# Kernel optimization log

Hardware: AMD Instinct MI355X
Metric: run time of the kernel (lower is better)

## Reference

```python
import jax, jax.numpy as jnp
import numpy as np

B, Q, C_IN, C_OUT, S, NH = 4, 4096, 256, 256, 8, 8
H_FEAT, W_FEAT = 128, 128


def grid_sample_bilinear(img, grid):
    """torch.nn.functional.grid_sample, mode='bilinear', padding_mode='zeros', align_corners=False.
    img: [B, C, H, W]; grid: [B, Hg, Wg, 2] with (x, y) in [-1, 1]. Returns [B, C, Hg, Wg]."""
    b, c, h, w = img.shape
    gx = (grid[..., 0] + 1.0) * (w * 0.5) - 0.5
    gy = (grid[..., 1] + 1.0) * (h * 0.5) - 0.5
    x0f = jnp.floor(gx)
    y0f = jnp.floor(gy)
    x0 = x0f.astype(jnp.int32)
    y0 = y0f.astype(jnp.int32)
    wx1 = (gx - x0f)[:, None]  # [B,1,Hg,Wg]
    wy1 = (gy - y0f)[:, None]
    img_flat = img.reshape(b, c, h * w)

    def corner(xi, yi):
        inb = ((xi >= 0) & (xi < w) & (yi >= 0) & (yi < h)).astype(img.dtype)
        idx = jnp.clip(yi, 0, h - 1) * w + jnp.clip(xi, 0, w - 1)
        v = jax.vmap(lambda im, ix: im[:, ix.reshape(-1)])(img_flat, idx)  # [B,C,Hg*Wg]
        return v.reshape(b, c, *xi.shape[1:]) * inb[:, None]

    v00 = corner(x0, y0)
    v01 = corner(x0 + 1, y0)
    v10 = corner(x0, y0 + 1)
    v11 = corner(x0 + 1, y0 + 1)
    return (v00 * (1 - wx1) * (1 - wy1) + v01 * wx1 * (1 - wy1)
            + v10 * (1 - wx1) * wy1 + v11 * wx1 * wy1)


def setup_inputs() -> dict:
    key = jax.random.key(0)
    ks = jax.random.split(key, 16)
    sc = 0.02
    return {
        "queries": jax.random.normal(ks[0], (B, Q, C_IN), jnp.float32),
        "keys": jax.random.normal(ks[1], (B, C_IN, H_FEAT, W_FEAT), jnp.float32),
        "values": jax.random.normal(ks[2], (B, C_IN, H_FEAT, W_FEAT), jnp.float32),
        "W_loc": jax.random.normal(ks[3], (C_IN, S * 2), jnp.float32) * sc,
        "b_loc": jnp.zeros((S * 2,), jnp.float32),
        "W_q": jax.random.normal(ks[4], (C_IN, C_OUT), jnp.float32) * sc,
        "b_q": jnp.zeros((C_OUT,), jnp.float32),
        "W_k": jax.random.normal(ks[5], (C_OUT, C_IN), jnp.float32) * sc,
        "b_k": jnp.zeros((C_OUT,), jnp.float32),
        "W_v": jax.random.normal(ks[6], (C_OUT, C_IN), jnp.float32) * sc,
        "b_v": jnp.zeros((C_OUT,), jnp.float32),
        "W_o": jax.random.normal(ks[7], (C_OUT, C_OUT), jnp.float32) * sc,
        "b_o": jnp.zeros((C_OUT,), jnp.float32),
    }


def reference(queries, keys, values, W_loc, b_loc, W_q, b_q, W_k, b_k, W_v, b_v, W_o, b_o):
    b, q, _ = queries.shape
    d = C_OUT // NH
    # predicted sampling locations in [-1, 1]: [B, Q, S, 2]
    loc = jnp.tanh(queries @ W_loc + b_loc).reshape(b, q, S, 2)
    # query projection -> [B, Q, NH, d]
    qh = (queries @ W_q + b_q).reshape(b, q, NH, d)
    # 1x1 conv projections of feature maps
    k_proj = jnp.einsum('oc,bchw->bohw', W_k, keys) + b_k[None, :, None, None]
    v_proj = jnp.einsum('oc,bchw->bohw', W_v, values) + b_v[None, :, None, None]
    # deformable sampling: [B, C_OUT, Q, S] -> [B, Q, NH, d, S]
    ks_ = grid_sample_bilinear(k_proj, loc).transpose(0, 2, 1, 3).reshape(b, q, NH, d, S)
    vs_ = grid_sample_bilinear(v_proj, loc).transpose(0, 2, 1, 3).reshape(b, q, NH, d, S)
    # per-query attention over S sampled points (note: scale uses full out_channels)
    attn = jnp.einsum('bqhd,bqhds->bqhs', qh, ks_) / np.sqrt(C_OUT).astype(np.float32)
    attn = jax.nn.softmax(attn, axis=-1)
    out = jnp.einsum('bqhds,bqhs->bqhd', vs_, attn).reshape(b, q, C_OUT)
    return out @ W_o + b_o
```

## Files before the change

kernel.cpp:

```cpp
#include <hip/hip_runtime.h>
#include <hip/hip_bf16.h>

#define NB 4
#define NQ 4096
#define CI 256
#define CO 256
#define NS 8
#define HFEAT 128
#define WFEAT 128
#define NPIX (HFEAT * WFEAT)

typedef short bf16x8 __attribute__((ext_vector_type(8)));
typedef float f32x4 __attribute__((ext_vector_type(4)));

__device__ __forceinline__ unsigned short f2b(float x) {
    union { float f; unsigned u; } v; v.f = x;
    unsigned r = v.u + 0x7fff + ((v.u >> 16) & 1);
    return (unsigned short)(r >> 16);
}
__device__ __forceinline__ float b2f(unsigned short x) {
    union { unsigned u; float f; } v; v.u = ((unsigned)x) << 16;
    return v.f;
}
__device__ __forceinline__ void b2f2(unsigned u, float& a, float& b) {
    union { unsigned x; float f; } va, vb;
    va.x = u << 16;
    vb.x = u & 0xffff0000u;
    a = va.f; b = vb.f;
}
__device__ __forceinline__ void gload16(const void* g, void* l) {
    __builtin_amdgcn_global_load_lds((const __attribute__((address_space(1))) void*)g,
                                     (__attribute__((address_space(3))) void*)l, 16, 0, 0);
}

__global__ __launch_bounds__(256) void k_prep_w(const float* __restrict__ Wk,
                                                const float* __restrict__ Wv,
                                                const float* __restrict__ Wq,
                                                const float* __restrict__ Wo,
                                                unsigned short* __restrict__ out) {
    int mat = blockIdx.y;
    int base = blockIdx.x * 1024 + threadIdx.x * 4;
    const float* src = (mat == 0) ? Wk : (mat == 1) ? Wv : (mat == 2) ? Wq : Wo;
    unsigned short* dst = out + (size_t)mat * 65536;
    if (mat < 2) {
#pragma unroll
        for (int i = 0; i < 4; ++i) dst[base + i] = f2b(src[base + i]);
    } else {
#pragma unroll
        for (int i = 0; i < 4; ++i) {
            int oi = base + i;
            int o = oi >> 8, c = oi & 255;
            dst[oi] = f2b(src[c * 256 + o]);
        }
    }
}

__global__ __launch_bounds__(256) void k_cvt(const float* __restrict__ in,
                                             unsigned short* __restrict__ out) {
    size_t i = ((size_t)blockIdx.x * 256 + threadIdx.x) * 8;
    float4 a = *reinterpret_cast<const float4*>(in + i);
    float4 b = *reinterpret_cast<const float4*>(in + i + 4);
    union { uint2 u2[2]; unsigned short h[8]; } pk;
    pk.h[0] = f2b(a.x); pk.h[1] = f2b(a.y); pk.h[2] = f2b(a.z); pk.h[3] = f2b(a.w);
    pk.h[4] = f2b(b.x); pk.h[5] = f2b(b.y); pk.h[6] = f2b(b.z); pk.h[7] = f2b(b.w);
    *reinterpret_cast<uint4*>(out + i) = *reinterpret_cast<uint4*>(&pk);
}

__global__ __launch_bounds__(256) void k_loc(const float* __restrict__ q,
                                             const float* __restrict__ Wl,
                                             const float* __restrict__ bl,
                                             float* __restrict__ loc) {
    __shared__ float qs[32][260];
    __shared__ float wlt[16][260];
    int t = threadIdx.x;
    int row0 = blockIdx.x * 32;
    {
        int rr = t >> 6;
        int c4 = (t & 63) * 4;
#pragma unroll
        for (int i = 0; i < 8; ++i) {
            int r = i * 4 + rr;
            *reinterpret_cast<float4*>(&qs[r][c4]) =
                *reinterpret_cast<const float4*>(q + (size_t)(row0 + r) * CI + c4);
        }
    }
    {
        int c = t;
#pragma unroll
        for (int col = 0; col < 16; ++col) wlt[col][c] = Wl[c * 16 + col];
    }
    __syncthreads();
    int r = t & 31;
    int cg = t >> 5;
    float a0 = bl[cg], a1 = bl[cg + 8];
    for (int c4 = 0; c4 < 256; c4 += 4) {
        float4 qv = *reinterpret_cast<const float4*>(&qs[r][c4]);
        float4 w0 = *reinterpret_cast<const float4*>(&wlt[cg][c4]);
        float4 w1 = *reinterpret_cast<const float4*>(&wlt[cg + 8][c4]);
        a0 = fmaf(qv.x, w0.x, a0); a0 = fmaf(qv.y, w0.y, a0);
        a0 = fmaf(qv.z, w0.z, a0); a0 = fmaf(qv.w, w0.w, a0);
        a1 = fmaf(qv.x, w1.x, a1); a1 = fmaf(qv.y, w1.y, a1);
        a1 = fmaf(qv.z, w1.z, a1); a1 = fmaf(qv.w, w1.w, a1);
    }
    loc[(size_t)(row0 + r) * 16 + cg] = tanhf(a0);
    loc[(size_t)(row0 + r) * 16 + cg + 8] = tanhf(a1);
}

template <int OUT_BF16>
__global__ __launch_bounds__(256) void k_gemm(const unsigned short* __restrict__ A,
                                              const unsigned short* __restrict__ Bt,
                                              const float* __restrict__ bias,
                                              void* __restrict__ outp) {
    __shared__ unsigned short As[128][32];
    __shared__ unsigned short Bs[128][32];
    int t = threadIdx.x;
    int w = t >> 6, l = t & 63;
    int bm = blockIdx.x >> 1, bc = blockIdx.x & 1;
    int m0 = bm * 128, n0 = bc * 128;
    int wr = w >> 1, wc = w & 1;

    f32x4 acc[4][4];
#pragma unroll
    for (int n = 0; n < 4; ++n) {
        float bv = bias[n0 + wc * 64 + n * 16 + (l & 15)];
#pragma unroll
        for (int m = 0; m < 4; ++m) acc[m][n] = f32x4{bv, bv, bv, bv};
    }

    int ar = wr * 64 + (l & 15);
    int br = wc * 64 + (l & 15);
    int kq = (l >> 4) * 8;
    int srow = (l >> 2);
    int scol = (l & 3) * 8;

    for (int kk = 0; kk < 8; ++kk) {
        int k0 = kk * 32;
#pragma unroll
        for (int j = 0; j < 2; ++j) {
            int row = w * 32 + j * 16 + srow;
            gload16(A + (size_t)(m0 + row) * CI + k0 + scol, &As[w * 32 + j * 16][0]);
            gload16(Bt + (size_t)(n0 + row) * CI + k0 + scol, &Bs[w * 32 + j * 16][0]);
        }
        __syncthreads();
        bf16x8 af[4], bfr[4];
#pragma unroll
        for (int m = 0; m < 4; ++m) af[m] = *reinterpret_cast<const bf16x8*>(&As[ar + m * 16][kq]);
#pragma unroll
        for (int n = 0; n < 4; ++n) bfr[n] = *reinterpret_cast<const bf16x8*>(&Bs[br + n * 16][kq]);
#pragma unroll
        for (int m = 0; m < 4; ++m)
#pragma unroll
            for (int n = 0; n < 4; ++n)
                acc[m][n] = __builtin_amdgcn_mfma_f32_16x16x32_bf16(af[m], bfr[n], acc[m][n], 0, 0, 0);
        __syncthreads();
    }

    int rbase = m0 + wr * 64 + (l >> 4) * 4;
    int cbase = n0 + wc * 64 + (l & 15);
#pragma unroll
    for (int m = 0; m < 4; ++m)
#pragma unroll
        for (int n = 0; n < 4; ++n)
#pragma unroll
            for (int r = 0; r < 4; ++r) {
                size_t row = rbase + m * 16 + r;
                size_t col = cbase + n * 16;
                if (OUT_BF16)
                    ((unsigned short*)outp)[row * CO + col] = f2b(acc[m][n][r]);
                else
                    ((float*)outp)[row * CO + col] = acc[m][n][r];
            }
}

__global__ __launch_bounds__(256) void k_proj(const float* __restrict__ keys,
                                              const float* __restrict__ values,
                                              const unsigned short* __restrict__ wbuf,
                                              const float* __restrict__ bK,
                                              const float* __restrict__ bV,
                                              unsigned short* __restrict__ kp,
                                              unsigned short* __restrict__ vp) {
    __shared__ unsigned short As[128][40];
    __shared__ unsigned short Bs[128][32];
    int blk = ((blockIdx.x & 7) << 8) | (blockIdx.x >> 3);
    int map = blk >> 10;
    int rem = blk & 1023;
    int b = rem >> 8;
    int rem2 = rem & 255;
    int pix0 = (rem2 >> 1) * 128;
    int o0 = (rem2 & 1) * 128;
    const float* X = (map ? values : keys) + (size_t)b * (CI * NPIX);
    const unsigned short* W = wbuf + (size_t)map * 65536;
    const float* bias = map ? bV : bK;
    unsigned short* outp = (map ? vp : kp) + (size_t)b * (NPIX * CO);

    int t = threadIdx.x;
    int w = t >> 6, l = t & 63;
    int wr = w >> 1, wc = w & 1;

    f32x4 acc[4][4];
#pragma unroll
    for (int n = 0; n < 4; ++n) {
        float bv = bias[o0 + wc * 64 + n * 16 + (l & 15)];
#pragma unroll
        for (int m = 0; m < 4; ++m) acc[m][n] = f32x4{bv, bv, bv, bv};
    }

    int srow = l >> 2, scol = (l & 3) * 8;
    int pl = t & 31;
    int ch = (t >> 5) * 2;
    int ar = wr * 64 + (l & 15);
    int br = wc * 64 + (l & 15);
    int kq = (l >> 4) * 8;

    for (int kk = 0; kk < 8; ++kk) {
        int k0 = kk * 32;
#pragma unroll
        for (int j = 0; j < 2; ++j) {
            int row = w * 32 + j * 16 + srow;
            gload16(W + (size_t)(o0 + row) * CI + k0 + scol, &Bs[w * 32 + j * 16][0]);
        }
        float v0[2][4], v1[2][4];
#pragma unroll
        for (int i = 0; i < 2; ++i) {
            const float* xr0 = X + (size_t)(k0 + i * 16 + ch) * NPIX + pix0 + pl;
            const float* xr1 = xr0 + NPIX;
#pragma unroll
            for (int j = 0; j < 4; ++j) {
                v0[i][j] = xr0[j * 32];
                v1[i][j] = xr1[j * 32];
            }
        }
#pragma unroll
        for (int i = 0; i < 2; ++i)
#pragma unroll
            for (int j = 0; j < 4; ++j) {
                unsigned pkd = (unsigned)f2b(v0[i][j]) | ((unsigned)f2b(v1[i][j]) << 16);
                *reinterpret_cast<unsigned*>(&As[pl + j * 32][i * 16 + ch]) = pkd;
            }
        __syncthreads();
        bf16x8 af[4], bfr[4];
#pragma unroll
        for (int m = 0; m < 4; ++m) af[m] = *reinterpret_cast<const bf16x8*>(&As[ar + m * 16][kq]);
#pragma unroll
        for (int n = 0; n < 4; ++n) bfr[n] = *reinterpret_cast<const bf16x8*>(&Bs[br + n * 16][kq]);
#pragma unroll
        for (int m = 0; m < 4; ++m)
#pragma unroll
            for (int n = 0; n < 4; ++n)
                acc[m][n] = __builtin_amdgcn_mfma_f32_16x16x32_bf16(af[m], bfr[n], acc[m][n], 0, 0, 0);
        __syncthreads();
    }

    int rbase = wr * 64 + (l >> 4) * 4;
    int cbase = o0 + wc * 64 + (l & 15);
#pragma unroll
    for (int m = 0; m < 4; ++m)
#pragma unroll
        for (int n = 0; n < 4; ++n)
#pragma unroll
            for (int r = 0; r < 4; ++r) {
                size_t row = (size_t)pix0 + rbase + m * 16 + r;
                size_t col = cbase + n * 16;
                outp[row * CO + col] = f2b(acc[m][n][r]);
            }
}

__global__ __launch_bounds__(256) void k_attn(const unsigned short* __restrict__ kp,
                                              const unsigned short* __restrict__ vp,
                                              const unsigned short* __restrict__ qh,
                                              const float* __restrict__ loc,
                                              unsigned short* __restrict__ aout) {
    int t = threadIdx.x;
    int wv = t >> 6, l = t & 63;
    int blk = blockIdx.x;
    int xcd = blk & 7;
    int b = xcd >> 1;
    int idx = ((blk >> 3) << 1) | (xcd & 1);
    int bq = (b << 12) | (idx << 2) | wv;

    float qv[4];
    {
        uint2 qr = *reinterpret_cast<const uint2*>(qh + (size_t)bq * CO + l * 4);
        b2f2(qr.x, qv[0], qv[1]);
        b2f2(qr.y, qv[2], qv[3]);
    }
    const unsigned short* kb = kp + (size_t)b * NPIX * CO;
    const unsigned short* vb = vp + (size_t)b * NPIX * CO;
    const float* lq = loc + (size_t)bq * (NS * 2);
    int choff = l * 4;

    float m = -3.0e38f, lsum = 0.f;
    float o0 = 0.f, o1 = 0.f, o2 = 0.f, o3 = 0.f;

#pragma unroll
    for (int s = 0; s < NS; ++s) {
        float x = lq[2 * s];
        float y = lq[2 * s + 1];
        float gx = (x + 1.f) * (WFEAT * 0.5f) - 0.5f;
        float gy = (y + 1.f) * (HFEAT * 0.5f) - 0.5f;
        float x0f = floorf(gx), y0f = floorf(gy);
        int x0 = (int)x0f, y0 = (int)y0f;
        float wx1 = gx - x0f, wy1 = gy - y0f;
        float wx0 = 1.f - wx1, wy0 = 1.f - wy1;
        bool xa = (x0 >= 0) && (x0 < WFEAT);
        bool xb = (x0 + 1 >= 0) && (x0 + 1 < WFEAT);
        bool ya = (y0 >= 0) && (y0 < HFEAT);
        bool yb = (y0 + 1 >= 0) && (y0 + 1 < HFEAT);
        size_t i00 = (size_t)(y0 * WFEAT + x0) * CO + choff;

        uint2 z = make_uint2(0u, 0u);
        uint2 k00 = z, k01 = z, k10 = z, k11 = z;
        uint2 v00 = z, v01 = z, v10 = z, v11 = z;
        if (xa && ya) { k00 = *(const uint2*)(kb + i00);                 v00 = *(const uint2*)(vb + i00); }
        if (xb && ya) { k01 = *(const uint2*)(kb + i00 + CO);            v01 = *(const uint2*)(vb + i00 + CO); }
        if (xa && yb) { k10 = *(const uint2*)(kb + i00 + WFEAT * CO);    v10 = *(const uint2*)(vb + i00 + WFEAT * CO); }
        if (xb && yb) { k11 = *(const uint2*)(kb + i00 + (WFEAT+1)*CO);  v11 = *(const uint2*)(vb + i00 + (WFEAT+1)*CO); }

        float a0, a1, b0, b1, c0, c1, d0, d1;
        float ks[4], vs[4];
        b2f2(k00.x, a0, a1); b2f2(k01.x, b0, b1); b2f2(k10.x, c0, c1); b2f2(k11.x, d0, d1);
        ks[0] = fmaf(fmaf(b0, wx1, a0 * wx0), wy0, fmaf(d0, wx1, c0 * wx0) * wy1);
        ks[1] = fmaf(fmaf(b1, wx1, a1 * wx0), wy0, fmaf(d1, wx1, c1 * wx0) * wy1);
        b2f2(k00.y, a0, a1); b2f2(k01.y, b0, b1); b2f2(k10.y, c0, c1); b2f2(k11.y, d0, d1);
        ks[2] = fmaf(fmaf(b0, wx1, a0 * wx0), wy0, fmaf(d0, wx1, c0 * wx0) * wy1);
        ks[3] = fmaf(fmaf(b1, wx1, a1 * wx0), wy0, fmaf(d1, wx1, c1 * wx0) * wy1);
        b2f2(v00.x, a0, a1); b2f2(v01.x, b0, b1); b2f2(v10.x, c0, c1); b2f2(v11.x, d0, d1);
        vs[0] = fmaf(fmaf(b0, wx1, a0 * wx0), wy0, fmaf(d0, wx1, c0 * wx0) * wy1);
        vs[1] = fmaf(fmaf(b1, wx1, a1 * wx0), wy0, fmaf(d1, wx1, c1 * wx0) * wy1);
        b2f2(v00.y, a0, a1); b2f2(v01.y, b0, b1); b2f2(v10.y, c0, c1); b2f2(v11.y, d0, d1);
        vs[2] = fmaf(fmaf(b0, wx1, a0 * wx0), wy0, fmaf(d0, wx1, c0 * wx0) * wy1);
        vs[3] = fmaf(fmaf(b1, wx1, a1 * wx0), wy0, fmaf(d1, wx1, c1 * wx0) * wy1);

        float p = fmaf(qv[0], ks[0], fmaf(qv[1], ks[1], fmaf(qv[2], ks[2], qv[3] * ks[3])));
        p += __shfl_xor(p, 1);
        p += __shfl_xor(p, 2);
        p += __shfl_xor(p, 4);
        float lg = p * 0.0625f;

        float nm = fmaxf(m, lg);
        float sc = __expf(m - nm);
        float wgt = __expf(lg - nm);
        lsum = fmaf(lsum, sc, wgt);
        o0 = fmaf(o0, sc, wgt * vs[0]);
        o1 = fmaf(o1, sc, wgt * vs[1]);
        o2 = fmaf(o2, sc, wgt * vs[2]);
        o3 = fmaf(o3, sc, wgt * vs[3]);
        m = nm;
    }

    float inv = 1.f / lsum;
    uint2 pk;
    pk.x = ((unsigned)f2b(o0 * inv)) | (((unsigned)f2b(o1 * inv)) << 16);
    pk.y = ((unsigned)f2b(o2 * inv)) | (((unsigned)f2b(o3 * inv)) << 16);
    *reinterpret_cast<uint2*>(aout + (size_t)bq * CO + choff) = pk;
}

extern "C" void kernel_launch(void* const* d_in, const int* in_sizes, int n_in,
                              void* d_out, int out_size, void* d_ws, size_t ws_size,
                              hipStream_t stream) {
    (void)in_sizes; (void)n_in; (void)out_size; (void)ws_size;
    const float* queries = (const float*)d_in[0];
    const float* keys    = (const float*)d_in[1];
    const float* values  = (const float*)d_in[2];
    const float* W_loc   = (const float*)d_in[3];
    const float* b_loc   = (const float*)d_in[4];
    const float* W_q     = (const float*)d_in[5];
    const float* b_q     = (const float*)d_in[6];
    const float* W_k     = (const float*)d_in[7];
    const float* b_k     = (const float*)d_in[8];
    const float* W_v     = (const float*)d_in[9];
    const float* b_v     = (const float*)d_in[10];
    const float* W_o     = (const float*)d_in[11];
    const float* b_o     = (const float*)d_in[12];
    float* out = (float*)d_out;

    char* ws = (char*)d_ws;
    unsigned short* kp   = (unsigned short*)(ws);
    unsigned short* vp   = (unsigned short*)(ws + 33554432);
    unsigned short* qbf  = (unsigned short*)(ws + 67108864);
    unsigned short* aout = (unsigned short*)(ws + 67108864);
    unsigned short* qh   = (unsigned short*)(ws + 75497472);
    float* locb          = (float*)(ws + 83886080);
    unsigned short* wbuf = (unsigned short*)(ws + 84934656);

    k_prep_w<<<dim3(64, 4), 256, 0, stream>>>(W_k, W_v, W_q, W_o, wbuf);
    k_cvt<<<dim3(2048), 256, 0, stream>>>(queries, qbf);
    k_loc<<<dim3(512), 256, 0, stream>>>(queries, W_loc, b_loc, locb);
    k_gemm<1><<<dim3(256), 256, 0, stream>>>(qbf, wbuf + 131072, b_q, qh);
    k_proj<<<dim3(2048), 256, 0, stream>>>(keys, values, wbuf, b_k, b_v, kp, vp);
    k_attn<<<dim3(NB * NQ / 4), 256, 0, stream>>>(kp, vp, qh, locb, aout);
    k_gemm<0><<<dim3(256), 256, 0, stream>>>(aout, wbuf + 196608, b_o, out);
}
```

Measured before the change: 128.3 us.

## Software-pipeline projection GEMM loads with double-buffered B tile and swizzled A layout

```diff
diff --git a/kernel.cpp b/kernel.cpp
--- a/kernel.cpp
+++ b/kernel.cpp
@@ -180,7 +180,7 @@
                                               unsigned short* __restrict__ kp,
                                               unsigned short* __restrict__ vp) {
     __shared__ unsigned short As[128][40];
-    __shared__ unsigned short Bs[128][32];
+    __shared__ unsigned short Bs[2][128][32];
     int blk = ((blockIdx.x & 7) << 8) | (blockIdx.x >> 3);
     int map = blk >> 10;
     int rem = blk & 1023;
@@ -205,50 +205,86 @@
         for (int m = 0; m < 4; ++m) acc[m][n] = f32x4{bv, bv, bv, bv};
     }
 
+    int cp0 = t >> 5;
+    int pxl = 4 * (t & 31);
+    int fx = ((t & 31) ^ ((t & 31) >> 2)) & 3;
+    int colA = cp0 ^ (fx << 2);
+    int colB = (cp0 + 8) ^ (fx << 2);
+    const float* Xp = X + pix0 + pxl;
+
     int srow = l >> 2, scol = (l & 3) * 8;
-    int pl = t & 31;
-    int ch = (t >> 5) * 2;
+
     int ar = wr * 64 + (l & 15);
     int br = wc * 64 + (l & 15);
-    int kq = (l >> 4) * 8;
+    int g = l >> 4;
+    int kq = g * 8;
+
+    float4 fa0, fa1, fa2, fa3;
+
+#define LOADA(kk)                                                         \
+    {                                                                     \
+        const float* p_ = Xp + (size_t)((kk) * 32 + 2 * cp0) * NPIX;      \
+        fa0 = *(const float4*)(p_);                                       \
+        fa1 = *(const float4*)(p_ + NPIX);                                \
+        fa2 = *(const float4*)(p_ + 16 * NPIX);                           \
+        fa3 = *(const float4*)(p_ + 17 * NPIX);                           \
+    }
+#define WRITEA()                                                          \
+    {                                                                     \
+        const float* q0_ = (const float*)&fa0;                            \
+        const float* q1_ = (const float*)&fa1;                            \
+        const float* q2_ = (const float*)&fa2;                            \
+        const float* q3_ = (const float*)&fa3;                            \
+        _Pragma("unroll")                                                 \
+        for (int j = 0; j < 4; ++j) {                                     \
+            unsigned d0_ = (unsigned)f2b(q0_[j]) | ((unsigned)f2b(q1_[j]) << 16); \
+            unsigned d1_ = (unsigned)f2b(q2_[j]) | ((unsigned)f2b(q3_[j]) << 16); \
+            unsigned* rp_ = (unsigned*)&As[pxl + j][0];                   \
+            rp_[colA] = d0_;                                              \
+            rp_[colB] = d1_;                                              \
+        }                                                                 \
+    }
+#define LOADB(kk, buf)                                                    \
+    {                                                                     \
+        int k0_ = (kk) * 32;                                              \
+        _Pragma("unroll")                                                 \
+        for (int j = 0; j < 2; ++j) {                                     \
+            int row_ = w * 32 + j * 16;                                   \
+            gload16(W + (size_t)(o0 + row_ + srow) * CI + k0_ + scol,     \
+                    &Bs[buf][row_][0]);                                   \
+        }                                                                 \
+    }
+
+    LOADA(0);
+    LOADB(0, 0);
+    WRITEA();
+    __syncthreads();
 
     for (int kk = 0; kk < 8; ++kk) {
-        int k0 = kk * 32;
-#pragma unroll
-        for (int j = 0; j < 2; ++j) {
-            int row = w * 32 + j * 16 + srow;
-            gload16(W + (size_t)(o0 + row) * CI + k0 + scol, &Bs[w * 32 + j * 16][0]);
-        }
-        float v0[2][4], v1[2][4];
-#pragma unroll
-        for (int i = 0; i < 2; ++i) {
-            const float* xr0 = X + (size_t)(k0 + i * 16 + ch) * NPIX + pix0 + pl;
-            const float* xr1 = xr0 + NPIX;
-#pragma unroll
-            for (int j = 0; j < 4; ++j) {
-                v0[i][j] = xr0[j * 32];
-                v1[i][j] = xr1[j * 32];
-            }
-        }
-#pragma unroll
-        for (int i = 0; i < 2; ++i)
-#pragma unroll
-            for (int j = 0; j < 4; ++j) {
-                unsigned pkd = (unsigned)f2b(v0[i][j]) | ((unsigned)f2b(v1[i][j]) << 16);
-                *reinterpret_cast<unsigned*>(&As[pl + j * 32][i * 16 + ch]) = pkd;
-            }
-        __syncthreads();
+        if (kk < 7) {
+            LOADA(kk + 1);
+            LOADB(kk + 1, (kk + 1) & 1);
+        }
         bf16x8 af[4], bfr[4];
 #pragma unroll
-        for (int m = 0; m < 4; ++m) af[m] = *reinterpret_cast<const bf16x8*>(&As[ar + m * 16][kq]);
-#pragma unroll
-        for (int n = 0; n < 4; ++n) bfr[n] = *reinterpret_cast<const bf16x8*>(&Bs[br + n * 16][kq]);
+        for (int m = 0; m < 4; ++m) {
+            int p = ar + m * 16;
+            int gm = (g ^ (((p >> 2) ^ (p >> 4)) & 3)) * 8;
+            af[m] = *reinterpret_cast<const bf16x8*>(&As[p][gm]);
+        }
+#pragma unroll
+        for (int n = 0; n < 4; ++n)
+            bfr[n] = *reinterpret_cast<const bf16x8*>(&Bs[kk & 1][br + n * 16][kq]);
 #pragma unroll
         for (int m = 0; m < 4; ++m)
 #pragma unroll
             for (int n = 0; n < 4; ++n)
                 acc[m][n] = __builtin_amdgcn_mfma_f32_16x16x32_bf16(af[m], bfr[n], acc[m][n], 0, 0, 0);
         __syncthreads();
+        if (kk < 7) {
+            WRITEA();
+            __syncthreads();
+        }
     }
 
     int rbase = wr * 64 + (l >> 4) * 4;
@@ -263,6 +299,9 @@
                 size_t col = cbase + n * 16;
                 outp[row * CO + col] = f2b(acc[m][n][r]);
             }
+#undef LOADA
+#undef WRITEA
+#undef LOADB
 }
 
 __global__ __launch_bounds__(256) void k_attn(const unsigned short* __restrict__ kp,
```

New measurement: 124.2 us. 3.1% less time.

## Restructure k_proj to stage full-K pixel tile once and reuse across both output halves

Applied to the files above, without the earlier changes.

```diff
diff --git a/kernel.cpp b/kernel.cpp
--- a/kernel.cpp
+++ b/kernel.cpp
@@ -27,6 +27,11 @@
     va.x = u << 16;
     vb.x = u & 0xffff0000u;
     a = va.f; b = vb.f;
+}
+__device__ __forceinline__ unsigned cvtpk(float a, float b) {
+    unsigned r;
+    asm("v_cvt_pk_bf16_f32 %0, %1, %2" : "=v"(r) : "v"(a), "v"(b));
+    return r;
 }
 __device__ __forceinline__ void gload16(const void* g, void* l) {
     __builtin_amdgcn_global_load_lds((const __attribute__((address_space(1))) void*)g,
@@ -172,22 +177,22 @@
             }
 }
 
-__global__ __launch_bounds__(256) void k_proj(const float* __restrict__ keys,
-                                              const float* __restrict__ values,
-                                              const unsigned short* __restrict__ wbuf,
-                                              const float* __restrict__ bK,
-                                              const float* __restrict__ bV,
-                                              unsigned short* __restrict__ kp,
-                                              unsigned short* __restrict__ vp) {
-    __shared__ unsigned short As[128][40];
-    __shared__ unsigned short Bs[128][32];
-    int blk = ((blockIdx.x & 7) << 8) | (blockIdx.x >> 3);
-    int map = blk >> 10;
-    int rem = blk & 1023;
-    int b = rem >> 8;
-    int rem2 = rem & 255;
-    int pix0 = (rem2 >> 1) * 128;
-    int o0 = (rem2 & 1) * 128;
+__global__ __launch_bounds__(256, 1) void k_proj(const float* __restrict__ keys,
+                                                 const float* __restrict__ values,
+                                                 const unsigned short* __restrict__ wbuf,
+                                                 const float* __restrict__ bK,
+                                                 const float* __restrict__ bV,
+                                                 unsigned short* __restrict__ kp,
+                                                 unsigned short* __restrict__ vp) {
+    __shared__ unsigned short As[128][264];
+    __shared__ unsigned short Bs[128][256];
+
+    int bid = blockIdx.x;
+    int map = bid >> 9;
+    int b = (bid >> 7) & 3;
+    int tile = bid & 127;
+    int pix0 = tile << 7;
+
     const float* X = (map ? values : keys) + (size_t)b * (CI * NPIX);
     const unsigned short* W = wbuf + (size_t)map * 65536;
     const float* bias = map ? bV : bK;
@@ -197,72 +202,124 @@
     int w = t >> 6, l = t & 63;
     int wr = w >> 1, wc = w & 1;
 
-    f32x4 acc[4][4];
-#pragma unroll
-    for (int n = 0; n < 4; ++n) {
-        float bv = bias[o0 + wc * 64 + n * 16 + (l & 15)];
-#pragma unroll
-        for (int m = 0; m < 4; ++m) acc[m][n] = f32x4{bv, bv, bv, bv};
-    }
-
-    int srow = l >> 2, scol = (l & 3) * 8;
-    int pl = t & 31;
-    int ch = (t >> 5) * 2;
+#define STAGEB(o0h)                                                          \
+    {                                                                        \
+        _Pragma("unroll")                                                    \
+        for (int j = 0; j < 16; ++j) {                                       \
+            int row0_ = w * 32 + 2 * j;                                      \
+            int rowl_ = row0_ + (l >> 5);                                    \
+            const unsigned short* src_ =                                     \
+                W + (size_t)((o0h) + rowl_) * CI + (((l & 31) ^ (rowl_ & 7)) << 3); \
+            gload16(src_, &Bs[row0_][0]);                                    \
+        }                                                                    \
+    }
+
+    int px = t & 31;
+    int cg = t >> 5;
+    int swA = ((px >> 3) & 1) << 2;
+    const float* Xb = X + pix0 + px;
+
+    float bufA[32], bufB[32];
+
+#define LOADC(buf, chunk)                                                    \
+    {                                                                        \
+        _Pragma("unroll")                                                    \
+        for (int cc = 0; cc < 8; ++cc) {                                     \
+            const float* p_ = Xb + (size_t)((chunk)*64 + cg * 8 + cc) * NPIX;\
+            _Pragma("unroll")                                                \
+            for (int w4 = 0; w4 < 4; ++w4) buf[cc * 4 + w4] = p_[w4 * 32];   \
+        }                                                                    \
+    }
+#define WRITEC(buf, chunk)                                                   \
+    {                                                                        \
+        _Pragma("unroll")                                                    \
+        for (int c2 = 0; c2 < 4; ++c2) {                                     \
+            _Pragma("unroll")                                                \
+            for (int w4 = 0; w4 < 4; ++w4) {                                 \
+                unsigned d_ = cvtpk(buf[(2 * c2) * 4 + w4], buf[(2 * c2 + 1) * 4 + w4]); \
+                ((unsigned*)&As[px + 32 * w4][0])[((chunk)*32 + cg * 4 + c2) ^ swA] = d_; \
+            }                                                                \
+        }                                                                    \
+    }
+
+    STAGEB(0);
+    LOADC(bufA, 0);
+    LOADC(bufB, 1);
+    WRITEC(bufA, 0);
+    LOADC(bufA, 2);
+    WRITEC(bufB, 1);
+    LOADC(bufB, 3);
+    WRITEC(bufA, 2);
+    WRITEC(bufB, 3);
+    __syncthreads();
+
     int ar = wr * 64 + (l & 15);
     int br = wc * 64 + (l & 15);
-    int kq = (l >> 4) * 8;
-
-    for (int kk = 0; kk < 8; ++kk) {
-        int k0 = kk * 32;
-#pragma unroll
-        for (int j = 0; j < 2; ++j) {
-            int row = w * 32 + j * 16 + srow;
-            gload16(W + (size_t)(o0 + row) * CI + k0 + scol, &Bs[w * 32 + j * 16][0]);
-        }
-        float v0[2][4], v1[2][4];
-#pragma unroll
-        for (int i = 0; i < 2; ++i) {
-            const float* xr0 = X + (size_t)(k0 + i * 16 + ch) * NPIX + pix0 + pl;
-            const float* xr1 = xr0 + NPIX;
-#pragma unroll
-            for (int j = 0; j < 4; ++j) {
-                v0[i][j] = xr0[j * 32];
-                v1[i][j] = xr1[j * 32];
-            }
-        }
-#pragma unroll
-        for (int i = 0; i < 2; ++i)
-#pragma unroll
-            for (int j = 0; j < 4; ++j) {
-                unsigned pkd = (unsigned)f2b(v0[i][j]) | ((unsigned)f2b(v1[i][j]) << 16);
-                *reinterpret_cast<unsigned*>(&As[pl + j * 32][i * 16 + ch]) = pkd;
-            }
-        __syncthreads();
-        bf16x8 af[4], bfr[4];
-#pragma unroll
-        for (int m = 0; m < 4; ++m) af[m] = *reinterpret_cast<const bf16x8*>(&As[ar + m * 16][kq]);
-#pragma unroll
-        for (int n = 0; n < 4; ++n) bfr[n] = *reinterpret_cast<const bf16x8*>(&Bs[br + n * 16][kq]);
-#pragma unroll
-        for (int m = 0; m < 4; ++m)
-#pragma unroll
-            for (int n = 0; n < 4; ++n)
-                acc[m][n] = __builtin_amdgcn_mfma_f32_16x16x32_bf16(af[m], bfr[n], acc[m][n], 0, 0, 0);
-        __syncthreads();
-    }
-
-    int rbase = wr * 64 + (l >> 4) * 4;
-    int cbase = o0 + wc * 64 + (l & 15);
-#pragma unroll
-    for (int m = 0; m < 4; ++m)
-#pragma unroll
-        for (int n = 0; n < 4; ++n)
-#pragma unroll
-            for (int r = 0; r < 4; ++r) {
-                size_t row = (size_t)pix0 + rbase + m * 16 + r;
-                size_t col = cbase + n * 16;
-                outp[row * CO + col] = f2b(acc[m][n][r]);
-            }
+    int g = l >> 4;
+    int aswS = ((l >> 3) & 1) << 3;
+
+    f32x4 acc[4][4];
+
+#define INITACC(o0h)                                                         \
+    {                                                                        \
+        _Pragma("unroll")                                                    \
+        for (int n = 0; n < 4; ++n) {                                        \
+            float bv_ = bias[(o0h) + wc * 64 + n * 16 + (l & 15)];           \
+            _Pragma("unroll")                                                \
+            for (int m = 0; m < 4; ++m) acc[m][n] = f32x4{bv_, bv_, bv_, bv_}; \
+        }                                                                    \
+    }
+#define COMPUTE()                                                            \
+    {                                                                        \
+        _Pragma("unroll")                                                    \
+        for (int kk = 0; kk < 8; ++kk) {                                     \
+            bf16x8 af[4], bfr[4];                                            \
+            _Pragma("unroll")                                                \
+            for (int m = 0; m < 4; ++m)                                      \
+                af[m] = *reinterpret_cast<const bf16x8*>(                    \
+                    &As[ar + m * 16][(kk * 32 + g * 8) ^ aswS]);             \
+            _Pragma("unroll")                                                \
+            for (int n = 0; n < 4; ++n)                                      \
+                bfr[n] = *reinterpret_cast<const bf16x8*>(                   \
+                    &Bs[br + n * 16][((kk * 4 + g) ^ (l & 7)) << 3]);        \
+            _Pragma("unroll")                                                \
+            for (int m = 0; m < 4; ++m)                                      \
+                _Pragma("unroll")                                            \
+                for (int n = 0; n < 4; ++n)                                  \
+                    acc[m][n] = __builtin_amdgcn_mfma_f32_16x16x32_bf16(     \
+                        af[m], bfr[n], acc[m][n], 0, 0, 0);                  \
+        }                                                                    \
+    }
+#define STOREC(o0h)                                                          \
+    {                                                                        \
+        int rb_ = wr * 64 + (l >> 4) * 4;                                    \
+        int cb_ = (o0h) + wc * 64 + (l & 15);                                \
+        _Pragma("unroll")                                                    \
+        for (int m = 0; m < 4; ++m)                                          \
+            _Pragma("unroll")                                                \
+            for (int n = 0; n < 4; ++n)                                      \
+                _Pragma("unroll")                                            \
+                for (int r = 0; r < 4; ++r)                                  \
+                    outp[(size_t)(pix0 + rb_ + m * 16 + r) * CO + cb_ + n * 16] = \
+                        f2b(acc[m][n][r]);                                   \
+    }
+
+    INITACC(0);
+    COMPUTE();
+    __syncthreads();
+    STAGEB(128);
+    STOREC(0);
+    INITACC(128);
+    __syncthreads();
+    COMPUTE();
+    STOREC(128);
+
+#undef STAGEB
+#undef LOADC
+#undef WRITEC
+#undef INITACC
+#undef COMPUTE
+#undef STOREC
 }
 
 __global__ __launch_bounds__(256) void k_attn(const unsigned short* __restrict__ kp,
@@ -387,7 +444,7 @@
     k_cvt<<<dim3(2048), 256, 0, stream>>>(queries, qbf);
     k_loc<<<dim3(512), 256, 0, stream>>>(queries, W_loc, b_loc, locb);
     k_gemm<1><<<dim3(256), 256, 0, stream>>>(qbf, wbuf + 131072, b_q, qh);
-    k_proj<<<dim3(2048), 256, 0, stream>>>(keys, values, wbuf, b_k, b_v, kp, vp);
+    k_proj<<<dim3(1024), 256, 0, stream>>>(keys, values, wbuf, b_k, b_v, kp, vp);
     k_attn<<<dim3(NB * NQ / 4), 256, 0, stream>>>(kp, vp, qh, locb, aout);
     k_gemm<0><<<dim3(256), 256, 0, stream>>>(aout, wbuf + 196608, b_o, out);
 }
```

Measured after the change: 138.9 us. 8.3% more time.

## Split feature-map projection into transpose-convert pass plus generic bf16 GEMM

Applied to the files above, without the earlier changes.

```diff
diff --git a/kernel.cpp b/kernel.cpp
--- a/kernel.cpp
+++ b/kernel.cpp
@@ -27,6 +27,11 @@
     va.x = u << 16;
     vb.x = u & 0xffff0000u;
     a = va.f; b = vb.f;
+}
+__device__ __forceinline__ unsigned cvtpk(float a, float b) {
+    unsigned r;
+    asm("v_cvt_pk_bf16_f32 %0, %1, %2" : "=v"(r) : "v"(a), "v"(b));
+    return r;
 }
 __device__ __forceinline__ void gload16(const void* g, void* l) {
     __builtin_amdgcn_global_load_lds((const __attribute__((address_space(1))) void*)g,
@@ -106,6 +111,38 @@
     loc[(size_t)(row0 + r) * 16 + cg + 8] = tanhf(a1);
 }
 
+__global__ __launch_bounds__(256) void k_tc(const float* __restrict__ X,
+                                            unsigned short* __restrict__ Xt) {
+    __shared__ float tile[64][256];
+    int bid = blockIdx.x;
+    int pt = bid & 63;
+    int cq = (bid >> 6) & 3;
+    int b = bid >> 8;
+    int px0 = pt << 8;
+    int c0 = cq << 6;
+
+    int t = threadIdx.x;
+    int w = t >> 6, l = t & 63;
+
+    const float* src = X + ((size_t)b * CI + c0 + w * 16) * NPIX + px0 + l * 4;
+#pragma unroll
+    for (int j = 0; j < 16; ++j) {
+        gload16(src + (size_t)j * NPIX, &tile[w * 16 + j][0]);
+    }
+    __syncthreads();
+
+    unsigned short* dst = Xt + ((size_t)b * NPIX + px0 + t) * CI + c0;
+#pragma unroll
+    for (int h = 0; h < 8; ++h) {
+        uint4 pk;
+        pk.x = cvtpk(tile[h * 8 + 0][t], tile[h * 8 + 1][t]);
+        pk.y = cvtpk(tile[h * 8 + 2][t], tile[h * 8 + 3][t]);
+        pk.z = cvtpk(tile[h * 8 + 4][t], tile[h * 8 + 5][t]);
+        pk.w = cvtpk(tile[h * 8 + 6][t], tile[h * 8 + 7][t]);
+        *reinterpret_cast<uint4*>(dst + h * 8) = pk;
+    }
+}
+
 template <int OUT_BF16>
 __global__ __launch_bounds__(256) void k_gemm(const unsigned short* __restrict__ A,
                                               const unsigned short* __restrict__ Bt,
@@ -169,99 +206,6 @@
                     ((unsigned short*)outp)[row * CO + col] = f2b(acc[m][n][r]);
                 else
                     ((float*)outp)[row * CO + col] = acc[m][n][r];
-            }
-}
-
-__global__ __launch_bounds__(256) void k_proj(const float* __restrict__ keys,
-                                              const float* __restrict__ values,
-                                              const unsigned short* __restrict__ wbuf,
-                                              const float* __restrict__ bK,
-                                              const float* __restrict__ bV,
-                                              unsigned short* __restrict__ kp,
-                                              unsigned short* __restrict__ vp) {
-    __shared__ unsigned short As[128][40];
-    __shared__ unsigned short Bs[128][32];
-    int blk = ((blockIdx.x & 7) << 8) | (blockIdx.x >> 3);
-    int map = blk >> 10;
-    int rem = blk & 1023;
-    int b = rem >> 8;
-    int rem2 = rem & 255;
-    int pix0 = (rem2 >> 1) * 128;
-    int o0 = (rem2 & 1) * 128;
-    const float* X = (map ? values : keys) + (size_t)b * (CI * NPIX);
-    const unsigned short* W = wbuf + (size_t)map * 65536;
-    const float* bias = map ? bV : bK;
-    unsigned short* outp = (map ? vp : kp) + (size_t)b * (NPIX * CO);
-
-    int t = threadIdx.x;
-    int w = t >> 6, l = t & 63;
-    int wr = w >> 1, wc = w & 1;
-
-    f32x4 acc[4][4];
-#pragma unroll
-    for (int n = 0; n < 4; ++n) {
-        float bv = bias[o0 + wc * 64 + n * 16 + (l & 15)];
-#pragma unroll
-        for (int m = 0; m < 4; ++m) acc[m][n] = f32x4{bv, bv, bv, bv};
-    }
-
-    int srow = l >> 2, scol = (l & 3) * 8;
-    int pl = t & 31;
-    int ch = (t >> 5) * 2;
-    int ar = wr * 64 + (l & 15);
-    int br = wc * 64 + (l & 15);
-    int kq = (l >> 4) * 8;
-
-    for (int kk = 0; kk < 8; ++kk) {
-        int k0 = kk * 32;
-#pragma unroll
-        for (int j = 0; j < 2; ++j) {
-            int row = w * 32 + j * 16 + srow;
-            gload16(W + (size_t)(o0 + row) * CI + k0 + scol, &Bs[w * 32 + j * 16][0]);
-        }
-        float v0[2][4], v1[2][4];
-#pragma unroll
-        for (int i = 0; i < 2; ++i) {
-            const float* xr0 = X + (size_t)(k0 + i * 16 + ch) * NPIX + pix0 + pl;
-            const float* xr1 = xr0 + NPIX;
-#pragma unroll
-            for (int j = 0; j < 4; ++j) {
-                v0[i][j] = xr0[j * 32];
-                v1[i][j] = xr1[j * 32];
-            }
-        }
-#pragma unroll
-        for (int i = 0; i < 2; ++i)
-#pragma unroll
-            for (int j = 0; j < 4; ++j) {
-                unsigned pkd = (unsigned)f2b(v0[i][j]) | ((unsigned)f2b(v1[i][j]) << 16);
-                *reinterpret_cast<unsigned*>(&As[pl + j * 32][i * 16 + ch]) = pkd;
-            }
-        __syncthreads();
-        bf16x8 af[4], bfr[4];
-#pragma unroll
-        for (int m = 0; m < 4; ++m) af[m] = *reinterpret_cast<const bf16x8*>(&As[ar + m * 16][kq]);
-#pragma unroll
-        for (int n = 0; n < 4; ++n) bfr[n] = *reinterpret_cast<const bf16x8*>(&Bs[br + n * 16][kq]);
-#pragma unroll
-        for (int m = 0; m < 4; ++m)
-#pragma unroll
-            for (int n = 0; n < 4; ++n)
-                acc[m][n] = __builtin_amdgcn_mfma_f32_16x16x32_bf16(af[m], bfr[n], acc[m][n], 0, 0, 0);
-        __syncthreads();
-    }
-
-    int rbase = wr * 64 + (l >> 4) * 4;
-    int cbase = o0 + wc * 64 + (l & 15);
-#pragma unroll
-    for (int m = 0; m < 4; ++m)
-#pragma unroll
-        for (int n = 0; n < 4; ++n)
-#pragma unroll
-            for (int r = 0; r < 4; ++r) {
-                size_t row = (size_t)pix0 + rbase + m * 16 + r;
-                size_t col = cbase + n * 16;
-                outp[row * CO + col] = f2b(acc[m][n][r]);
             }
 }
 
@@ -377,17 +321,23 @@
     char* ws = (char*)d_ws;
     unsigned short* kp   = (unsigned short*)(ws);
     unsigned short* vp   = (unsigned short*)(ws + 33554432);
-    unsigned short* qbf  = (unsigned short*)(ws + 67108864);
-    unsigned short* aout = (unsigned short*)(ws + 67108864);
-    unsigned short* qh   = (unsigned short*)(ws + 75497472);
-    float* locb          = (float*)(ws + 83886080);
-    unsigned short* wbuf = (unsigned short*)(ws + 84934656);
+    unsigned short* Xt   = (unsigned short*)(ws + 67108864);
+    unsigned short* qbf  = (unsigned short*)(ws + 100663296);
+    unsigned short* aout = (unsigned short*)(ws + 100663296);
+    unsigned short* qh   = (unsigned short*)(ws + 109051904);
+    float* locb          = (float*)(ws + 117440512);
+    unsigned short* wbuf = (unsigned short*)(ws + 118489088);
 
     k_prep_w<<<dim3(64, 4), 256, 0, stream>>>(W_k, W_v, W_q, W_o, wbuf);
     k_cvt<<<dim3(2048), 256, 0, stream>>>(queries, qbf);
     k_loc<<<dim3(512), 256, 0, stream>>>(queries, W_loc, b_loc, locb);
     k_gemm<1><<<dim3(256), 256, 0, stream>>>(qbf, wbuf + 131072, b_q, qh);
-    k_proj<<<dim3(2048), 256, 0, stream>>>(keys, values, wbuf, b_k, b_v, kp, vp);
+
+    k_tc<<<dim3(1024), 256, 0, stream>>>(keys, Xt);
+    k_gemm<1><<<dim3(1024), 256, 0, stream>>>(Xt, wbuf, b_k, kp);
+    k_tc<<<dim3(1024), 256, 0, stream>>>(values, Xt);
+    k_gemm<1><<<dim3(1024), 256, 0, stream>>>(Xt, wbuf + 65536, b_v, vp);
+
     k_attn<<<dim3(NB * NQ / 4), 256, 0, stream>>>(kp, vp, qh, locb, aout);
     k_gemm<0><<<dim3(256), 256, 0, stream>>>(aout, wbuf + 196608, b_o, out);
 }
```

Measured after the change: 176.1 us. 37.3% more time.
